# Performance work log

Hardware: AMD Instinct MI355X
Metric: run time of the kernel (lower is better)

## Reference

```python
import jax, jax.numpy as jnp
import numpy as np

B, L, D, H = 4, 2048, 256, 512


def silu_backward(x):
    s = jax.nn.silu(x)
    return s + jax.nn.sigmoid(x) * (1.0 - s)


def setup_inputs() -> dict:
    key = jax.random.key(0)
    ks = jax.random.split(key, 12)
    sc = 0.02
    return {
        "x": jax.random.normal(ks[0], (B, L, D), jnp.float32),
        "W1": jax.random.normal(ks[1], (B, H, D), jnp.float32) * sc,
        "W2": jax.random.normal(ks[2], (B, D, H), jnp.float32) * sc,
        "Wq": jax.random.normal(ks[3], (D, D), jnp.float32) * sc,
        "bq": jnp.zeros((D,), jnp.float32),
        "Wk": jax.random.normal(ks[4], (D, D), jnp.float32) * sc,
        "bk": jnp.zeros((D,), jnp.float32),
        "Wv": jax.random.normal(ks[5], (D, D), jnp.float32) * sc,
        "bv": jnp.zeros((D,), jnp.float32),
        "w_lr": jax.random.normal(ks[6], (D,), jnp.float32) * sc,
        "b_lr": jnp.zeros((), jnp.float32),
        "w_wd": jax.random.normal(ks[7], (D,), jnp.float32) * sc,
        "b_wd": jnp.zeros((), jnp.float32),
        "log_base_lr": jnp.asarray(np.log(0.1), jnp.float32),
        "log_base_wd": jnp.asarray(np.log(0.5), jnp.float32),
    }


def reference(x, W1, W2, Wq, bq, Wk, bk, Wv, bv, w_lr, b_lr, w_wd, b_wd, log_base_lr, log_base_wd):
    b, l, d = x.shape
    query = x @ Wq + bq
    key = x @ Wk + bk
    value = x @ Wv + bv
    lr = jnp.exp(log_base_lr) * jax.nn.sigmoid(x @ w_lr + b_lr)          # [b,l]
    log_wd = jnp.log(1.0 - jnp.exp(log_base_wd) * jax.nn.sigmoid(x @ w_wd + b_wd))  # [b,l]

    wd_cross = jnp.exp(jnp.cumsum(log_wd, axis=1))                       # [b,l]
    idx = jnp.arange(l)
    strict_upper = idx[:, None] < idx[None, :]                           # (m, j): j > m
    A = jnp.where(strict_upper[None], log_wd[:, None, :], 0.0)           # [b,m,j]
    wd_inner = jnp.exp(jnp.cumsum(A, axis=2)) * (idx[:, None] <= idx[None, :])[None]  # [b,m,j]

    X1 = key
    Z1 = jnp.einsum('bhd,bld->blh', W1, X1)
    X2 = jax.nn.silu(Z1)
    Z2 = jnp.einsum('bdh,blh->bld', W2, X2)
    grad_Z2 = Z2 - value
    grad_X2 = jnp.einsum('bdh,bld->blh', W2, grad_Z2)
    grad_Z1 = silu_backward(Z1) * grad_X2

    X1_ = query
    mask_X1X1_ = jnp.einsum('bld,bmd->blm', X1, X1_) * wd_inner
    Z1_inner = -jnp.einsum('blh,bl,blm->bmh', grad_Z1, lr, mask_X1X1_)
    Z1_cross = jnp.einsum('bhd,bld,bl->blh', W1, X1_, wd_cross)
    Z1_ = Z1_inner + Z1_cross

    W1_next = (-jnp.einsum('blh,bl,bld->bhd', grad_Z1, lr * wd_inner[:, :, -1], X1)
               + W1 * wd_cross[:, -1][:, None, None])

    X2_ = jax.nn.silu(Z1_)
    mask_X2X2_ = jnp.einsum('blh,bmh->blm', X2, X2_) * wd_inner
    Z2_inner = -jnp.einsum('bld,bl,blm->bmd', grad_Z2, lr, mask_X2X2_)
    Z2_cross = jnp.einsum('bdh,blh,bl->bld', W2, X2_, wd_cross)
    Z2_ = Z2_inner + Z2_cross

    W2_next = (-jnp.einsum('bld,bl,blh->bdh', grad_Z2, lr * wd_inner[:, :, -1], X2)
               + W2 * wd_cross[:, -1][:, None, None])

    return (Z2_, W1_next, W2_next)
```

## Files before the change

kernel.cpp:

```cpp
#include <hip/hip_runtime.h>

typedef __bf16 bf16;
typedef __bf16 bf16x8 __attribute__((ext_vector_type(8)));
typedef __bf16 bf16x4 __attribute__((ext_vector_type(4)));
typedef float  f32x4  __attribute__((ext_vector_type(4)));

#define SB 72
#define CUTOFF -18.0

__device__ __forceinline__ float silu_f(float x){
  float s = 1.f/(1.f+__expf(-x));
  return x*s;
}
__device__ __forceinline__ float silu_bwd_f(float x){
  float s = 1.f/(1.f+__expf(-x));
  float si = x*s;
  return si + s*(1.f-si);
}

struct MArgs {
  const bf16* A; const bf16* B;
  long sA, sB;
  int lda, ldb;
  int M, N, K;
  int mode;
  float* Cf; long sCf;
  bf16*  Cb; long sCb;
  bf16*  Cb2; long sCb2;
  bf16*  Ct;  long sCt;  int ldct;
  bf16*  Ct2; long sCt2;
  int ldc;
  const float* auxf; int ldax; long sAuxf;
  const bf16*  auxb; long sAuxb;
  const float* rowv; long sRowv;
  const float* rowv2; long sRowv2;
  const double* cd;  long sCd;
  const float* clp;  long sClp;
  bf16* Q; bf16* Ko; float* Vo; const float* bqkv;
};

template<int TM>
__device__ __forceinline__ void gemm_body(const MArgs& g, int bm, int bn, int bz)
{
  constexpr int TTP = (TM==64) ? 72 : 136;
  __shared__ __align__(16) bf16 sh[(TM+64)*SB];
  bf16* As = sh;
  bf16* Bs = sh + TM*SB;

  const int row0 = bm*TM, col0 = bn*64;
  constexpr int NI  = TM/32;
  constexpr int TPR = 256/TM;
  constexpr int EPR = 64/TPR;
  constexpr int NCH = EPR/8;

  const bf16* A = g.A + (long)bz*g.sA;
  const bf16* B = g.B + (long)bz*g.sB;
  const double* cd = g.cd ? g.cd + (long)bz*g.sCd : (const double*)0;
  float* Cf = g.Cf ? g.Cf + (long)bz*g.sCf : (float*)0;
  bf16* Cb  = g.Cb ? g.Cb + (long)bz*g.sCb : (bf16*)0;
  bf16* Cb2 = g.Cb2 ? g.Cb2 + (long)bz*g.sCb2 : (bf16*)0;
  bf16* Ct  = g.Ct ? g.Ct + (long)bz*g.sCt : (bf16*)0;
  bf16* Ct2 = g.Ct2 ? g.Ct2 + (long)bz*g.sCt2 : (bf16*)0;
  const float* auxf = g.auxf ? g.auxf + (long)bz*g.sAuxf : (const float*)0;
  const bf16*  auxb = g.auxb ? g.auxb + (long)bz*g.sAuxb : (const bf16*)0;
  const float* rowv = g.rowv ? g.rowv + (long)bz*g.sRowv : (const float*)0;
  const float* rowv2 = g.rowv2 ? g.rowv2 + (long)bz*g.sRowv2 : (const float*)0;

  const int tid = threadIdx.x;
  const int mode = g.mode;
  const int lane = tid & 63;
  const int w = tid >> 6;
  const int wr = (w >> 1) * (TM/2), wc = (w & 1) * 32;
  const int l15 = lane & 15;
  const int quad = lane >> 4;

  f32x4 acc[NI][2];
  #pragma unroll
  for (int i=0;i<NI;i++)
    #pragma unroll
    for (int j=0;j<2;j++)
      #pragma unroll
      for (int r=0;r<4;r++) acc[i][j][r] = 0.f;

  const int rowA = tid / TPR, kA = (tid % TPR) * EPR;
  const int rowB = tid >> 2,  kB = (tid & 3) * 16;

  int klo = 0;
  if (cd) {
    const double cref = cd[g.K-1];
    while (klo + 64 < g.K && (cref - cd[klo+63]) < CUTOFF) klo += 64;
  }

  for (int k0 = klo; k0 < g.K; k0 += 64) {
    {
      const bf16* s = A + (long)(row0+rowA)*g.lda + k0 + kA;
      #pragma unroll
      for (int p=0;p<NCH;p++)
        *(bf16x8*)&As[rowA*SB + kA + p*8] = *(const bf16x8*)(s + p*8);
    }
    {
      const bf16* s = B + (long)(col0+rowB)*g.ldb + k0 + kB;
      *(bf16x8*)&Bs[rowB*SB + kB]     = *(const bf16x8*)s;
      *(bf16x8*)&Bs[rowB*SB + kB + 8] = *(const bf16x8*)(s+8);
    }
    __syncthreads();
    #pragma unroll
    for (int ch=0; ch<2; ch++){
      bf16x8 af[NI], bf2[2];
      #pragma unroll
      for (int i=0;i<NI;i++) af[i]  = *(const bf16x8*)&As[(wr + i*16 + l15)*SB + ch*32 + quad*8];
      #pragma unroll
      for (int j=0;j<2;j++) bf2[j] = *(const bf16x8*)&Bs[(wc + j*16 + l15)*SB + ch*32 + quad*8];
      #pragma unroll
      for (int i=0;i<NI;i++)
        #pragma unroll
        for (int j=0;j<2;j++)
          acc[i][j] = __builtin_amdgcn_mfma_f32_16x16x32_bf16(af[i], bf2[j], acc[i][j], 0, 0, 0);
    }
    __syncthreads();
  }

  float clv = 0.f;
  if (mode == 10) clv = *(g.clp + (long)bz*g.sClp);

  const bool hasT = (TM==64) ? (mode==1 || mode==2 || mode==3)
                             : (mode==11 && col0 >= 256 && col0 < 512);

  #pragma unroll
  for (int i=0;i<NI;i++){
    const int rb = row0 + wr + i*16 + quad*4;
    const int rloc = wr + i*16 + quad*4;
    #pragma unroll
    for (int j=0;j<2;j++){
      const int c = col0 + wc + j*16 + l15;
      const int cloc = wc + j*16 + l15;
      bf16 tv[4], tv2[4]; bool doT = false, doT2 = false;
      #pragma unroll
      for (int reg=0; reg<4; reg++){
        const int r = rb + reg;
        float v = acc[i][j][reg];
        const long co = (long)r*g.ldc + c;
        switch (mode) {
          case 1: {
            Cb[co]  = (bf16)v;
            float sv = silu_f(v);
            Cb2[co] = (bf16)sv;
            tv[reg] = (bf16)(sv * rowv[r]); doT = true;
          } break;
          case 2: {
            bf16 o = (bf16)(v - auxf[(long)r*g.ldax + c]);
            Cb[co] = o; tv[reg] = o; doT = true;
          } break;
          case 3: {
            float v3 = silu_bwd_f((float)auxb[(long)r*g.ldax + c]) * v * rowv[r];
            tv[reg]  = (bf16)v3;
            tv2[reg] = (bf16)(v3 * rowv2[r]);
            doT = true; doT2 = true;
          } break;
          case 10: {
            Cf[co] = v + auxf[(long)r*g.ldax + c]*clv;
          } break;
          case 11: {
            float o = v + g.bqkv[c];
            if (c < 256)      g.Q [(long)r*256 + c]       = (bf16)o;
            else if (c < 512) { g.Ko[(long)r*256 + (c-256)] = (bf16)o; tv[reg] = (bf16)o; doT = true; }
            else              g.Vo[(long)r*256 + (c-512)] = o;
          } break;
        }
      }
      if (hasT && doT) {
        bf16x4 t4 = { tv[0], tv[1], tv[2], tv[3] };
        *(bf16x4*)&sh[cloc*TTP + rloc] = t4;
        if (doT2) {
          bf16x4 t4b = { tv2[0], tv2[1], tv2[2], tv2[3] };
          *(bf16x4*)&sh[64*72 + cloc*TTP + rloc] = t4b;
        }
      }
    }
  }

  if (hasT) {
    __syncthreads();
    if constexpr (TM == 64) {
      const int cl = tid >> 2, rl = (tid & 3)*16;
      bf16x8 u0 = *(const bf16x8*)&sh[cl*72 + rl];
      bf16x8 u1 = *(const bf16x8*)&sh[cl*72 + rl + 8];
      bf16* d = Ct + (long)(col0+cl)*g.ldct + row0 + rl;
      *(bf16x8*)d       = u0;
      *(bf16x8*)(d + 8) = u1;
      if (mode == 3) {
        bf16x8 v0 = *(const bf16x8*)&sh[64*72 + cl*72 + rl];
        bf16x8 v1 = *(const bf16x8*)&sh[64*72 + cl*72 + rl + 8];
        bf16* d2 = Ct2 + (long)(col0+cl)*g.ldct + row0 + rl;
        *(bf16x8*)d2       = v0;
        *(bf16x8*)(d2 + 8) = v1;
      }
    } else {
      const int cl = tid >> 2, rl = (tid & 3)*32;
      const int b = row0 / g.ldct, l0r = row0 % g.ldct;
      bf16* d = Ct + (long)b*g.sCt + (long)(col0-256+cl)*g.ldct + l0r + rl;
      #pragma unroll
      for (int p=0;p<4;p++)
        *(bf16x8*)(d + p*8) = *(const bf16x8*)&sh[cl*136 + rl + p*8];
    }
  }
}

__global__ __launch_bounds__(256)
void mfma_gemm128(MArgs g){ gemm_body<128>(g, blockIdx.x, blockIdx.y, blockIdx.z); }

__global__ __launch_bounds__(256)
void mfma_gemm64(MArgs g){ gemm_body<64>(g, blockIdx.x, blockIdx.y, blockIdx.z); }

__global__ __launch_bounds__(256)
void wnext_gemm(MArgs g1, MArgs g2){
  const int z = blockIdx.z;
  const MArgs& g = (z < 4) ? g1 : g2;
  const int bz = z & 3;
  if ((int)blockIdx.x*128 >= g.M || (int)blockIdx.y*64 >= g.N) return;
  gemm_body<128>(g, blockIdx.x, blockIdx.y, bz);
}

struct PArgs {
  const bf16 *A, *B1;
  long sA, sB1;
  const double* cd; long sCd;
  const float* lrv; long sLr;
  bf16* P;
};

template<int KS64, int ISLR>
__global__ __launch_bounds__(256)
void pgen(PArgs g)
{
  const int mt = blockIdx.x, slot = blockIdx.y, bz = blockIdx.z;
  const int m0 = mt*64;
  const int l0 = (m0 & ~127) - slot*128;
  if (l0 < 0) return;
  const double* cd = g.cd + (long)bz*g.sCd;
  const int lref = (l0+127 < m0) ? (l0+127) : m0;
  if (cd[m0] - cd[lref] < CUTOFF) return;

  const int K1 = KS64*64;
  const bf16* A  = g.A  + (long)bz*g.sA;
  const bf16* B1 = g.B1 + (long)bz*g.sB1;
  const float* lrv = ISLR ? (g.lrv + (long)bz*g.sLr) : (const float*)0;

  const int tid = threadIdx.x;
  const int lane = tid & 63, w = tid >> 6;
  const int wr = (w>>1)*32, wc = (w&1)*64;
  const int l15 = lane & 15, quad = lane >> 4;
  const int rowA = tid >> 2, kA = (tid & 3) * 16;
  const int rowB = tid >> 1, kB = (tid & 1) * 32;

  __shared__ __align__(16) bf16 As[64*SB];
  __shared__ __align__(16) bf16 Bs[128*SB];

  f32x4 O[2][4];
  #pragma unroll
  for (int i=0;i<2;i++)
    #pragma unroll
    for (int j=0;j<4;j++)
      #pragma unroll
      for (int r=0;r<4;r++) O[i][j][r] = 0.f;

  for (int ks=0; ks<KS64; ks++){
    const int k0 = ks*64;
    {
      const bf16* s = A + (long)(m0+rowA)*K1 + k0 + kA;
      *(bf16x8*)&As[rowA*SB + kA]     = *(const bf16x8*)s;
      *(bf16x8*)&As[rowA*SB + kA + 8] = *(const bf16x8*)(s+8);
    }
    {
      const bf16* s = B1 + (long)(l0+rowB)*K1 + k0 + kB;
      #pragma unroll
      for (int p=0;p<4;p++) *(bf16x8*)&Bs[rowB*SB + kB + p*8] = *(const bf16x8*)(s + p*8);
    }
    __syncthreads();
    #pragma unroll
    for (int ch=0; ch<2; ch++){
      bf16x8 af[2], bfr[4];
      #pragma unroll
      for (int i=0;i<2;i++) af[i]  = *(const bf16x8*)&As[(wr + i*16 + l15)*SB + ch*32 + quad*8];
      #pragma unroll
      for (int j=0;j<4;j++) bfr[j] = *(const bf16x8*)&Bs[(wc + j*16 + l15)*SB + ch*32 + quad*8];
      #pragma unroll
      for (int i=0;i<2;i++)
        #pragma unroll
        for (int j=0;j<4;j++)
          O[i][j] = __builtin_amdgcn_mfma_f32_16x16x32_bf16(af[i], bfr[j], O[i][j], 0, 0, 0);
    }
    __syncthreads();
  }

  bf16* Pt = g.P + (((long)bz*32 + mt)*3 + slot) * (64*128);
  float cl[4], lv[4];
  #pragma unroll
  for (int j=0;j<4;j++){
    const int l = l0 + wc + j*16 + l15;
    cl[j] = (float)cd[l];
    if (ISLR) lv[j] = lrv[l];
  }
  #pragma unroll
  for (int i=0;i<2;i++)
    #pragma unroll
    for (int reg=0; reg<4; reg++){
      const int mloc = wr + i*16 + quad*4 + reg;
      const int m = m0 + mloc;
      const float cm = (float)cd[m];
      #pragma unroll
      for (int j=0;j<4;j++){
        const int lloc = wc + j*16 + l15;
        const int l = l0 + lloc;
        float v = -O[i][j][reg] * __expf(cm - cl[j]);
        if (ISLR) v *= lv[j];
        if (l > m) v = 0.f;
        Pt[mloc*128 + lloc] = (bf16)v;
      }
    }
}

struct CArgs {
  const bf16 *A, *W, *P, *B2;
  long sA, sW, sB2;
  int ldb2;
  const double* cd; long sCd;
  const float* wdc; long sWdc;
  float* Cf; long sCf;
  bf16* Cb; long sCb;
  int ldc;
};

template<int KS64, int SILU, int ZSPLIT>
__global__ __launch_bounds__(256)
void cons(CArgs g)
{
  const int mt = blockIdx.x;
  const int m0 = mt*64, n0 = blockIdx.y*64;
  const int bz   = ZSPLIT ? (blockIdx.z >> 1) : blockIdx.z;
  const int half = ZSPLIT ? (blockIdx.z & 1)  : 0;
  const int K1 = KS64*64;
  const bf16* A  = g.A  + (long)bz*g.sA;
  const bf16* W  = g.W  + (long)bz*g.sW;
  const bf16* B2 = g.B2 + (long)bz*g.sB2;
  const double* cd = g.cd + (long)bz*g.sCd;
  const float* wdc = g.wdc + (long)bz*g.sWdc;

  const int tid = threadIdx.x;
  const int lane = tid & 63, w = tid >> 6;
  const int wr = (w>>1)*32, wc = (w&1)*32;
  const int l15 = lane & 15, quad = lane >> 4;
  const int rowA = tid >> 2, kA = (tid & 3) * 16;

  bool alive[3];
  int nalive = 0;
  #pragma unroll
  for (int s=0;s<3;s++){
    const int l0 = (m0 & ~127) - s*128;
    bool a = (l0 >= 0);
    if (a) {
      const int lref = (l0+127 < m0) ? (l0+127) : m0;
      a = (cd[m0] - cd[lref] >= CUTOFF);
    }
    alive[s] = a; nalive += a ? 1 : 0;
  }
  if (ZSPLIT && half == 1 && nalive == 0) return;

  __shared__ __align__(16) bf16 As[64*SB];
  __shared__ __align__(16) bf16 Bs[64*SB];

  f32x4 O[2][2];
  #pragma unroll
  for (int i=0;i<2;i++)
    #pragma unroll
    for (int j=0;j<2;j++)
      #pragma unroll
      for (int r=0;r<4;r++) O[i][j][r] = 0.f;

  if (half == 0) {
    for (int ks=0; ks<KS64; ks++){
      const int k0 = ks*64;
      {
        const bf16* s = A + (long)(m0+rowA)*K1 + k0 + kA;
        *(bf16x8*)&As[rowA*SB + kA]     = *(const bf16x8*)s;
        *(bf16x8*)&As[rowA*SB + kA + 8] = *(const bf16x8*)(s+8);
      }
      {
        const bf16* s = W + (long)(n0+rowA)*K1 + k0 + kA;
        *(bf16x8*)&Bs[rowA*SB + kA]     = *(const bf16x8*)s;
        *(bf16x8*)&Bs[rowA*SB + kA + 8] = *(const bf16x8*)(s+8);
      }
      __syncthreads();
      #pragma unroll
      for (int ch=0; ch<2; ch++){
        bf16x8 af[2], bfr[2];
        #pragma unroll
        for (int i=0;i<2;i++) af[i]  = *(const bf16x8*)&As[(wr + i*16 + l15)*SB + ch*32 + quad*8];
        #pragma unroll
        for (int j=0;j<2;j++) bfr[j] = *(const bf16x8*)&Bs[(wc + j*16 + l15)*SB + ch*32 + quad*8];
        #pragma unroll
        for (int i=0;i<2;i++)
          #pragma unroll
          for (int j=0;j<2;j++)
            O[i][j] = __builtin_amdgcn_mfma_f32_16x16x32_bf16(af[i], bfr[j], O[i][j], 0, 0, 0);
      }
      __syncthreads();
    }
    #pragma unroll
    for (int i=0;i<2;i++)
      #pragma unroll
      for (int reg=0; reg<4; reg++){
        const float s = wdc[m0 + wr + i*16 + quad*4 + reg];
        #pragma unroll
        for (int j=0;j<2;j++) O[i][j][reg] *= s;
      }
  }

  if (!ZSPLIT || half == 1) {
    for (int s=0; s<3; s++){
      if (!alive[s]) continue;
      const int l0 = (m0 & ~127) - s*128;
      const bf16* Pt = g.P + (((long)bz*32 + mt)*3 + s) * (64*128);
      for (int hk=0; hk<2; hk++){
        {
          const bf16* sp = Pt + (long)rowA*128 + hk*64 + kA;
          *(bf16x8*)&As[rowA*SB + kA]     = *(const bf16x8*)sp;
          *(bf16x8*)&As[rowA*SB + kA + 8] = *(const bf16x8*)(sp+8);
        }
        {
          const bf16* sp = B2 + (long)(n0+rowA)*g.ldb2 + l0 + hk*64 + kA;
          *(bf16x8*)&Bs[rowA*SB + kA]     = *(const bf16x8*)sp;
          *(bf16x8*)&Bs[rowA*SB + kA + 8] = *(const bf16x8*)(sp+8);
        }
        __syncthreads();
        #pragma unroll
        for (int ch=0; ch<2; ch++){
          bf16x8 af[2], bfr[2];
          #pragma unroll
          for (int i=0;i<2;i++) af[i]  = *(const bf16x8*)&As[(wr + i*16 + l15)*SB + ch*32 + quad*8];
          #pragma unroll
          for (int j=0;j<2;j++) bfr[j] = *(const bf16x8*)&Bs[(wc + j*16 + l15)*SB + ch*32 + quad*8];
          #pragma unroll
          for (int i=0;i<2;i++)
            #pragma unroll
            for (int j=0;j<2;j++)
              O[i][j] = __builtin_amdgcn_mfma_f32_16x16x32_bf16(af[i], bfr[j], O[i][j], 0, 0, 0);
        }
        __syncthreads();
      }
    }
  }

  #pragma unroll
  for (int i=0;i<2;i++){
    const int rb = m0 + wr + i*16 + quad*4;
    #pragma unroll
    for (int j=0;j<2;j++){
      const int c = n0 + wc + j*16 + l15;
      #pragma unroll
      for (int reg=0; reg<4; reg++){
        const long co = (long)(rb+reg)*g.ldc + c;
        if (ZSPLIT)     unsafeAtomicAdd(&g.Cf[(long)bz*g.sCf + co], O[i][j][reg]);
        else if (SILU)  g.Cb[(long)bz*g.sCb + co] = (bf16)silu_f(O[i][j][reg]);
        else            g.Cf[(long)bz*g.sCf + co] = O[i][j][reg];
      }
    }
  }
}

struct FrontArgs {
  const float *x, *W1, *W2, *Wq, *Wk, *Wv;
  bf16 *xb, *W1b, *W2b, *Wqkvt, *W2t;
  float* out0;
  const float *wlr, *blr, *wwd, *bwd, *lbl, *lbw;
  float *lr, *lw;
  long LD4, HD4, HD;
};

__global__ __launch_bounds__(256)
void front_kernel(FrontArgs f)
{
  __shared__ bf16 t[64][72];
  const int bid = blockIdx.x;
  const int tid = threadIdx.x;

  if (bid < 1536) {
    const float* src; bf16* dst; long n; long base;
    if (bid < 1024)      { src = f.x;  dst = f.xb;  n = f.LD4; base = (long)bid*2048; }
    else if (bid < 1280) { src = f.W1; dst = f.W1b; n = f.HD4; base = (long)(bid-1024)*2048; }
    else                 { src = f.W2; dst = f.W2b; n = f.HD4; base = (long)(bid-1280)*2048; }
    long i = base + (long)tid*8;
    if (i >= n) return;
    float4 a = *(const float4*)&src[i];
    float4 b = *(const float4*)&src[i+4];
    bf16x8 o;
    o[0]=(bf16)a.x; o[1]=(bf16)a.y; o[2]=(bf16)a.z; o[3]=(bf16)a.w;
    o[4]=(bf16)b.x; o[5]=(bf16)b.y; o[6]=(bf16)b.z; o[7]=(bf16)b.w;
    *(bf16x8*)&dst[i] = o;
    return;
  }
  if (bid < 2560) {
    long i = (long)(bid-1536)*2048 + (long)tid*8;
    float4 z = {0.f,0.f,0.f,0.f};
    *(float4*)&f.out0[i]   = z;
    *(float4*)&f.out0[i+4] = z;
    return;
  }
  if (bid < 2736) {
    const float* ip; bf16* op; int R, C; int r0, c0;
    if (bid < 2608) {
      const int r = bid - 2560;
      const int z = r >> 4, rem = r & 15;
      ip = z==0 ? f.Wq : (z==1 ? f.Wk : f.Wv);
      op = f.Wqkvt + (long)z*256*256;
      R = 256; C = 256;
      r0 = (rem & 3)*64; c0 = (rem >> 2)*64;
    } else {
      const int r = bid - 2608;
      const int b = r >> 5, rem = r & 31;
      ip = f.W2 + (long)b*f.HD;
      op = f.W2t + (long)b*f.HD;
      R = 256; C = 512;
      r0 = (rem & 3)*64; c0 = (rem >> 2)*64;
    }
    const int lr_ = tid>>2, lc = (tid&3)*16;
    #pragma unroll
    for (int q=0;q<4;q++){
      float4 a = *(const float4*)&ip[(long)(r0+lr_)*C + c0+lc + q*4];
      t[lr_][lc+q*4+0] = (bf16)a.x; t[lr_][lc+q*4+1] = (bf16)a.y;
      t[lr_][lc+q*4+2] = (bf16)a.z; t[lr_][lc+q*4+3] = (bf16)a.w;
    }
    __syncthreads();
    const int oc = tid>>2, orr = (tid&3)*16;
    bf16x8 u, v;
    #pragma unroll
    for (int i=0;i<8;i++){ u[i] = t[orr+i][oc]; v[i] = t[orr+8+i][oc]; }
    *(bf16x8*)&op[(long)(c0+oc)*R + r0+orr]   = u;
    *(bf16x8*)&op[(long)(c0+oc)*R + r0+orr+8] = v;
    return;
  }
  {
    const int row  = (bid-2736)*4 + (tid >> 6);
    const int lane = tid & 63;
    const float4 a = ((const float4*)(f.x + (long)row*256))[lane];
    const float4 u = ((const float4*)f.wlr)[lane];
    const float4 w = ((const float4*)f.wwd)[lane];
    float d1 = a.x*u.x + a.y*u.y + a.z*u.z + a.w*u.w;
    float d2 = a.x*w.x + a.y*w.y + a.z*w.z + a.w*w.w;
    #pragma unroll
    for (int off=32; off; off>>=1) {
      d1 += __shfl_down(d1, off);
      d2 += __shfl_down(d2, off);
    }
    if (lane == 0) {
      float s1 = 1.f/(1.f+expf(-(d1 + f.blr[0])));
      f.lr[row] = expf(f.lbl[0]) * s1;
      float s2 = 1.f/(1.f+expf(-(d2 + f.bwd[0])));
      f.lw[row] = logf(1.f - expf(f.lbw[0]) * s2);
    }
  }
}

__global__ __launch_bounds__(256)
void cumsum_kernel(const float* __restrict__ lw, const float* __restrict__ lr,
                   double* __restrict__ cd, float* __restrict__ wdc,
                   float* __restrict__ se1, float* __restrict__ se2, int L,
                   const float* __restrict__ bq, const float* __restrict__ bk,
                   const float* __restrict__ bv, float* __restrict__ bqkv)
{
  const int b = blockIdx.x;
  const int t = threadIdx.x;
  if (b == 4) {
    for (int i = t; i < 768; i += 256)
      bqkv[i] = (i<256) ? bq[i] : ((i<512) ? bk[i-256] : bv[i-512]);
    return;
  }
  const float* lwb = lw + (long)b*L;
  __shared__ double sum_s[256];
  double loc[8];
  double s = 0.0;
  #pragma unroll
  for (int i=0;i<8;i++){ s += (double)lwb[t*8+i]; loc[i] = s; }
  sum_s[t] = s;
  __syncthreads();
  for (int off=1; off<256; off<<=1){
    double v = 0.0;
    if (t >= off) v = sum_s[t-off];
    __syncthreads();
    sum_s[t] += v;
    __syncthreads();
  }
  const double prefix = (t > 0) ? sum_s[t-1] : 0.0;
  const double total  = sum_s[255];
  #pragma unroll
  for (int i=0;i<8;i++){
    double c = prefix + loc[i];
    long idx = (long)b*L + t*8 + i;
    cd[idx]  = c;
    wdc[idx] = (float)exp(c);
    double e = exp(total - c);
    se1[idx] = (float)(-e);
    se2[idx] = (float)(-e) * lr[idx];
  }
}

extern "C" void kernel_launch(void* const* d_in, const int* in_sizes, int n_in,
                              void* d_out, int out_size, void* d_ws, size_t ws_size,
                              hipStream_t stream)
{
  const int Bn = 4, L = 2048, D = 256, H = 512;
  const long LD = (long)L*D, LH = (long)L*H, HD = (long)H*D;

  const float* x   = (const float*)d_in[0];
  const float* W1  = (const float*)d_in[1];
  const float* W2  = (const float*)d_in[2];
  const float* Wq  = (const float*)d_in[3];
  const float* bq  = (const float*)d_in[4];
  const float* Wk  = (const float*)d_in[5];
  const float* bk  = (const float*)d_in[6];
  const float* Wv  = (const float*)d_in[7];
  const float* bv  = (const float*)d_in[8];
  const float* wlr = (const float*)d_in[9];
  const float* blr = (const float*)d_in[10];
  const float* wwd = (const float*)d_in[11];
  const float* bwd = (const float*)d_in[12];
  const float* lbl = (const float*)d_in[13];
  const float* lbw = (const float*)d_in[14];
  (void)in_sizes; (void)n_in; (void)out_size; (void)ws_size;

  float* out0 = (float*)d_out;
  float* out1 = out0 + (long)Bn*LD;
  float* out2 = out1 + (long)Bn*HD;

  char* wsp = (char*)d_ws;
  size_t off = 0;
  auto alloc = [&](size_t bytes)->void*{
    void* p = wsp + off; off += (bytes + 255) & ~(size_t)255; return p;
  };
  bf16* xb    = (bf16*)alloc((size_t)Bn*LD*2);
  bf16* Wqkvt = (bf16*)alloc((size_t)3*D*D*2);
  float* bqkv = (float*)alloc((size_t)3*D*4);
  bf16* W1b  = (bf16*)alloc((size_t)Bn*HD*2);
  bf16* W2b  = (bf16*)alloc((size_t)Bn*HD*2);
  bf16* W2t  = (bf16*)alloc((size_t)Bn*HD*2);
  bf16* Qb   = (bf16*)alloc((size_t)Bn*LD*2);
  bf16* Kb   = (bf16*)alloc((size_t)Bn*LD*2);
  bf16* Kt   = (bf16*)alloc((size_t)Bn*LD*2);
  float* Vf  = (float*)alloc((size_t)Bn*LD*4);
  bf16* Z1b  = (bf16*)alloc((size_t)Bn*LH*2);
  bf16* X2b  = (bf16*)alloc((size_t)Bn*LH*2);
  bf16* X2t  = (bf16*)alloc((size_t)Bn*LH*2);
  bf16* gZb  = (bf16*)alloc((size_t)Bn*LD*2);
  bf16* gZt  = (bf16*)alloc((size_t)Bn*LD*2);
  bf16* A1t  = (bf16*)alloc((size_t)Bn*LH*2);
  bf16* A1s  = (bf16*)alloc((size_t)Bn*LH*2);
  bf16* X2_b = (bf16*)alloc((size_t)Bn*LH*2);
  bf16* Pb1  = (bf16*)alloc((size_t)Bn*32*3*64*128*2);
  bf16* Pb2  = (bf16*)alloc((size_t)Bn*32*3*64*128*2);
  float* lrb = (float*)alloc((size_t)Bn*L*4);
  float* lwb = (float*)alloc((size_t)Bn*L*4);
  float* wdc = (float*)alloc((size_t)Bn*L*4);
  float* se1 = (float*)alloc((size_t)Bn*L*4);
  float* se2 = (float*)alloc((size_t)Bn*L*4);
  double* cdb = (double*)alloc((size_t)Bn*L*8);

  auto run128 = [&](const MArgs& g, int Z){
    dim3 grid(g.M/128, g.N/64, Z);
    mfma_gemm128<<<grid, 256, 0, stream>>>(g);
  };
  auto run64 = [&](const MArgs& g, int Z){
    dim3 grid(g.M/64, g.N/64, Z);
    mfma_gemm64<<<grid, 256, 0, stream>>>(g);
  };

  {
    FrontArgs f{};
    f.x = x; f.W1 = W1; f.W2 = W2; f.Wq = Wq; f.Wk = Wk; f.Wv = Wv;
    f.xb = xb; f.W1b = W1b; f.W2b = W2b; f.Wqkvt = Wqkvt; f.W2t = W2t;
    f.out0 = out0;
    f.wlr = wlr; f.blr = blr; f.wwd = wwd; f.bwd = bwd; f.lbl = lbl; f.lbw = lbw;
    f.lr = lrb; f.lw = lwb;
    f.LD4 = Bn*LD; f.HD4 = Bn*HD; f.HD = HD;
    front_kernel<<<dim3(4784), 256, 0, stream>>>(f);
  }
  cumsum_kernel<<<dim3(5), 256, 0, stream>>>(lwb, lrb, cdb, wdc, se1, se2, L, bq, bk, bv, bqkv);

  {
    MArgs g{}; g.A = xb; g.lda = D; g.B = Wqkvt; g.ldb = D;
    g.M = Bn*L; g.N = 3*D; g.K = D; g.mode = 11; g.ldc = 0;
    g.Q = Qb; g.Ko = Kb; g.Vo = Vf; g.bqkv = bqkv;
    g.Ct = Kt; g.sCt = LD; g.ldct = L;
    run128(g, 1);
  }
  {
    MArgs g{}; g.A = Kb; g.lda = D; g.sA = LD; g.B = W1b; g.ldb = D; g.sB = HD;
    g.M = L; g.N = H; g.K = D; g.mode = 1; g.ldc = H;
    g.Cb = Z1b; g.sCb = LH; g.Cb2 = X2b; g.sCb2 = LH;
    g.Ct = X2t; g.sCt = LH; g.ldct = L;
    g.rowv = se2; g.sRowv = L;
    run64(g, Bn);
  }
  {
    MArgs g{}; g.A = X2b; g.lda = H; g.sA = LH; g.B = W2b; g.ldb = H; g.sB = HD;
    g.M = L; g.N = D; g.K = H; g.mode = 2; g.ldc = D;
    g.auxf = Vf; g.ldax = D; g.sAuxf = LD; g.Cb = gZb; g.sCb = LD;
    g.Ct = gZt; g.sCt = LD; g.ldct = L; run64(g, Bn);
  }
  {
    MArgs g{}; g.A = gZb; g.lda = D; g.sA = LD; g.B = W2t; g.ldb = D; g.sB = HD;
    g.M = L; g.N = H; g.K = D; g.mode = 3; g.ldc = H;
    g.auxb = Z1b; g.ldax = H; g.sAuxb = LH;
    g.rowv = lrb; g.sRowv = L; g.rowv2 = se1; g.sRowv2 = L;
    g.Ct = A1t; g.sCt = LH; g.ldct = L;
    g.Ct2 = A1s; g.sCt2 = LH;
    run64(g, Bn);
  }
  {
    PArgs p{};
    p.A = Qb; p.sA = LD; p.B1 = Kb; p.sB1 = LD;
    p.cd = cdb; p.sCd = L; p.P = Pb1;
    pgen<4,0><<<dim3(32,3,Bn), 256, 0, stream>>>(p);
  }
  {
    CArgs c{};
    c.A = Qb; c.sA = LD; c.W = W1b; c.sW = HD;
    c.P = Pb1; c.B2 = A1t; c.sB2 = LH; c.ldb2 = L;
    c.cd = cdb; c.sCd = L; c.wdc = wdc; c.sWdc = L;
    c.Cb = X2_b; c.sCb = LH; c.ldc = H;
    cons<4,1,0><<<dim3(32, H/64, Bn), 256, 0, stream>>>(c);
  }
  {
    PArgs p{};
    p.A = X2_b; p.sA = LH; p.B1 = X2b; p.sB1 = LH;
    p.cd = cdb; p.sCd = L; p.lrv = lrb; p.sLr = L; p.P = Pb2;
    pgen<8,1><<<dim3(32,3,Bn), 256, 0, stream>>>(p);
  }
  {
    CArgs c{};
    c.A = X2_b; c.sA = LH; c.W = W2b; c.sW = HD;
    c.P = Pb2; c.B2 = gZt; c.sB2 = LD; c.ldb2 = L;
    c.cd = cdb; c.sCd = L; c.wdc = wdc; c.sWdc = L;
    c.Cf = out0; c.sCf = LD; c.ldc = D;
    cons<8,0,1><<<dim3(32, D/64, Bn*2), 256, 0, stream>>>(c);
  }
  {
    MArgs g1{}; g1.A = A1s; g1.lda = L; g1.sA = LH; g1.B = Kt; g1.ldb = L; g1.sB = LD;
    g1.M = H; g1.N = D; g1.K = L; g1.mode = 10; g1.ldc = D;
    g1.cd = cdb; g1.sCd = L;
    g1.auxf = W1; g1.ldax = D; g1.sAuxf = HD; g1.clp = wdc + (L-1); g1.sClp = L;
    g1.Cf = out1; g1.sCf = HD;

    MArgs g2{}; g2.A = gZt; g2.lda = L; g2.sA = LD; g2.B = X2t; g2.ldb = L; g2.sB = LH;
    g2.M = D; g2.N = H; g2.K = L; g2.mode = 10; g2.ldc = H;
    g2.cd = cdb; g2.sCd = L;
    g2.auxf = W2; g2.ldax = H; g2.sAuxf = HD; g2.clp = wdc + (L-1); g2.sClp = L;
    g2.Cf = out2; g2.sCf = HD;

    wnext_gemm<<<dim3(4,8,8), 256, 0, stream>>>(g1, g2);
  }
}
```

Measured before the change: 232.3 us.

## Double-buffer LDS with register prefetch in GEMM kernels and retile W-next GEMM

The GEMM, pgen and cons kernels now use two LDS buffers with register prefetch of the next K-tiles, so global loads overlap MFMA compute and one barrier per step is dropped. The dead-chunk search for the decay cutoff becomes a wavefront ballot in place of a serial loop. The W-next GEMM switches from 128-row to 64-row tiles with double the grid to raise occupancy. In exchange LDS use doubles and register pressure rises, which may cut occupancy, and the reuse of a buffer two steps later relies on the intervening barrier for correctness.

Result: faster. 223.7 us (-3.7%).

```diff
diff --git a/kernel.cpp b/kernel.cpp
--- a/kernel.cpp
+++ b/kernel.cpp
@@ -43,9 +43,8 @@
 __device__ __forceinline__ void gemm_body(const MArgs& g, int bm, int bn, int bz)
 {
   constexpr int TTP = (TM==64) ? 72 : 136;
-  __shared__ __align__(16) bf16 sh[(TM+64)*SB];
-  bf16* As = sh;
-  bf16* Bs = sh + TM*SB;
+  constexpr int BUF = (TM+64)*SB;
+  __shared__ __align__(16) bf16 sh[2*BUF];
 
   const int row0 = bm*TM, col0 = bn*64;
   constexpr int NI  = TM/32;
@@ -88,22 +87,28 @@
   int klo = 0;
   if (cd) {
     const double cref = cd[g.K-1];
-    while (klo + 64 < g.K && (cref - cd[klo+63]) < CUTOFF) klo += 64;
-  }
-
-  for (int k0 = klo; k0 < g.K; k0 += 64) {
-    {
-      const bf16* s = A + (long)(row0+rowA)*g.lda + k0 + kA;
-      #pragma unroll
-      for (int p=0;p<NCH;p++)
-        *(bf16x8*)&As[rowA*SB + kA + p*8] = *(const bf16x8*)(s + p*8);
-    }
-    {
-      const bf16* s = B + (long)(col0+rowB)*g.ldb + k0 + kB;
-      *(bf16x8*)&Bs[rowB*SB + kB]     = *(const bf16x8*)s;
-      *(bf16x8*)&Bs[rowB*SB + kB + 8] = *(const bf16x8*)(s+8);
-    }
-    __syncthreads();
+    const int nch = g.K >> 6;
+    bool dead = (lane < nch-1) && ((cref - cd[lane*64+63]) < CUTOFF);
+    unsigned long long mask = __ballot(dead);
+    klo = (int)__builtin_ctzll(~mask) * 64;
+  }
+
+  const bf16* Abase = A + (long)(row0+rowA)*g.lda + kA;
+  const bf16* Bbase = B + (long)(col0+rowB)*g.ldb + kB;
+
+  bf16x8 paA[NCH], pbA0, pbA1, paB[NCH], pbB0, pbB1;
+  #pragma unroll
+  for (int p=0;p<NCH;p++) paA[p] = *(const bf16x8*)(Abase + klo + p*8);
+  pbA0 = *(const bf16x8*)(Bbase + klo);
+  pbA1 = *(const bf16x8*)(Bbase + klo + 8);
+  if (klo + 64 < g.K) {
+    #pragma unroll
+    for (int p=0;p<NCH;p++) paB[p] = *(const bf16x8*)(Abase + klo + 64 + p*8);
+    pbB0 = *(const bf16x8*)(Bbase + klo + 64);
+    pbB1 = *(const bf16x8*)(Bbase + klo + 64 + 8);
+  }
+
+  auto compute = [&](const bf16* As, const bf16* Bs){
     #pragma unroll
     for (int ch=0; ch<2; ch++){
       bf16x8 af[NI], bf2[2];
@@ -117,7 +122,39 @@
         for (int j=0;j<2;j++)
           acc[i][j] = __builtin_amdgcn_mfma_f32_16x16x32_bf16(af[i], bf2[j], acc[i][j], 0, 0, 0);
     }
-    __syncthreads();
+  };
+
+  for (int k0 = klo; k0 < g.K; k0 += 128) {
+    {
+      bf16* As = sh; bf16* Bs = sh + TM*SB;
+      #pragma unroll
+      for (int p=0;p<NCH;p++) *(bf16x8*)&As[rowA*SB + kA + p*8] = paA[p];
+      *(bf16x8*)&Bs[rowB*SB + kB]     = pbA0;
+      *(bf16x8*)&Bs[rowB*SB + kB + 8] = pbA1;
+      __syncthreads();
+      if (k0 + 128 < g.K) {
+        #pragma unroll
+        for (int p=0;p<NCH;p++) paA[p] = *(const bf16x8*)(Abase + k0 + 128 + p*8);
+        pbA0 = *(const bf16x8*)(Bbase + k0 + 128);
+        pbA1 = *(const bf16x8*)(Bbase + k0 + 128 + 8);
+      }
+      compute(As, Bs);
+    }
+    if (k0 + 64 < g.K) {
+      bf16* As = sh + BUF; bf16* Bs = sh + BUF + TM*SB;
+      #pragma unroll
+      for (int p=0;p<NCH;p++) *(bf16x8*)&As[rowA*SB + kA + p*8] = paB[p];
+      *(bf16x8*)&Bs[rowB*SB + kB]     = pbB0;
+      *(bf16x8*)&Bs[rowB*SB + kB + 8] = pbB1;
+      __syncthreads();
+      if (k0 + 192 < g.K) {
+        #pragma unroll
+        for (int p=0;p<NCH;p++) paB[p] = *(const bf16x8*)(Abase + k0 + 192 + p*8);
+        pbB0 = *(const bf16x8*)(Bbase + k0 + 192);
+        pbB1 = *(const bf16x8*)(Bbase + k0 + 192 + 8);
+      }
+      compute(As, Bs);
+    }
   }
 
   float clv = 0.f;
@@ -217,8 +254,8 @@
   const int z = blockIdx.z;
   const MArgs& g = (z < 4) ? g1 : g2;
   const int bz = z & 3;
-  if ((int)blockIdx.x*128 >= g.M || (int)blockIdx.y*64 >= g.N) return;
-  gemm_body<128>(g, blockIdx.x, blockIdx.y, bz);
+  if ((int)blockIdx.x*64 >= g.M || (int)blockIdx.y*64 >= g.N) return;
+  gemm_body<64>(g, blockIdx.x, blockIdx.y, bz);
 }
 
 struct PArgs {
@@ -253,8 +290,8 @@
   const int rowA = tid >> 2, kA = (tid & 3) * 16;
   const int rowB = tid >> 1, kB = (tid & 1) * 32;
 
-  __shared__ __align__(16) bf16 As[64*SB];
-  __shared__ __align__(16) bf16 Bs[128*SB];
+  constexpr int BUFP = (64+128)*SB;
+  __shared__ __align__(16) bf16 sh[2*BUFP];
 
   f32x4 O[2][4];
   #pragma unroll
@@ -264,19 +301,20 @@
       #pragma unroll
       for (int r=0;r<4;r++) O[i][j][r] = 0.f;
 
-  for (int ks=0; ks<KS64; ks++){
-    const int k0 = ks*64;
-    {
-      const bf16* s = A + (long)(m0+rowA)*K1 + k0 + kA;
-      *(bf16x8*)&As[rowA*SB + kA]     = *(const bf16x8*)s;
-      *(bf16x8*)&As[rowA*SB + kA + 8] = *(const bf16x8*)(s+8);
-    }
-    {
-      const bf16* s = B1 + (long)(l0+rowB)*K1 + k0 + kB;
-      #pragma unroll
-      for (int p=0;p<4;p++) *(bf16x8*)&Bs[rowB*SB + kB + p*8] = *(const bf16x8*)(s + p*8);
-    }
-    __syncthreads();
+  const bf16* Abase = A + (long)(m0+rowA)*K1 + kA;
+  const bf16* Bbase = B1 + (long)(l0+rowB)*K1 + kB;
+
+  bf16x8 paA0, paA1, pbA[4], paB0, paB1, pbB[4];
+  paA0 = *(const bf16x8*)Abase;
+  paA1 = *(const bf16x8*)(Abase + 8);
+  #pragma unroll
+  for (int p=0;p<4;p++) pbA[p] = *(const bf16x8*)(Bbase + p*8);
+  paB0 = *(const bf16x8*)(Abase + 64);
+  paB1 = *(const bf16x8*)(Abase + 64 + 8);
+  #pragma unroll
+  for (int p=0;p<4;p++) pbB[p] = *(const bf16x8*)(Bbase + 64 + p*8);
+
+  auto compute = [&](const bf16* As, const bf16* Bs){
     #pragma unroll
     for (int ch=0; ch<2; ch++){
       bf16x8 af[2], bfr[4];
@@ -290,7 +328,41 @@
         for (int j=0;j<4;j++)
           O[i][j] = __builtin_amdgcn_mfma_f32_16x16x32_bf16(af[i], bfr[j], O[i][j], 0, 0, 0);
     }
-    __syncthreads();
+  };
+
+  for (int ks=0; ks<KS64; ks+=2){
+    {
+      bf16* As = sh; bf16* Bs = sh + 64*SB;
+      *(bf16x8*)&As[rowA*SB + kA]     = paA0;
+      *(bf16x8*)&As[rowA*SB + kA + 8] = paA1;
+      #pragma unroll
+      for (int p=0;p<4;p++) *(bf16x8*)&Bs[rowB*SB + kB + p*8] = pbA[p];
+      __syncthreads();
+      if (ks+2 < KS64) {
+        const int kn = (ks+2)*64;
+        paA0 = *(const bf16x8*)(Abase + kn);
+        paA1 = *(const bf16x8*)(Abase + kn + 8);
+        #pragma unroll
+        for (int p=0;p<4;p++) pbA[p] = *(const bf16x8*)(Bbase + kn + p*8);
+      }
+      compute(As, Bs);
+    }
+    {
+      bf16* As = sh + BUFP; bf16* Bs = sh + BUFP + 64*SB;
+      *(bf16x8*)&As[rowA*SB + kA]     = paB0;
+      *(bf16x8*)&As[rowA*SB + kA + 8] = paB1;
+      #pragma unroll
+      for (int p=0;p<4;p++) *(bf16x8*)&Bs[rowB*SB + kB + p*8] = pbB[p];
+      __syncthreads();
+      if (ks+3 < KS64) {
+        const int kn = (ks+3)*64;
+        paB0 = *(const bf16x8*)(Abase + kn);
+        paB1 = *(const bf16x8*)(Abase + kn + 8);
+        #pragma unroll
+        for (int p=0;p<4;p++) pbB[p] = *(const bf16x8*)(Bbase + kn + p*8);
+      }
+      compute(As, Bs);
+    }
   }
 
   bf16* Pt = g.P + (((long)bz*32 + mt)*3 + slot) * (64*128);
@@ -366,8 +438,8 @@
   }
   if (ZSPLIT && half == 1 && nalive == 0) return;
 
-  __shared__ __align__(16) bf16 As[64*SB];
-  __shared__ __align__(16) bf16 Bs[64*SB];
+  constexpr int BUFC = 128*SB;
+  __shared__ __align__(16) bf16 sh[2*BUFC];
 
   f32x4 O[2][2];
   #pragma unroll
@@ -377,34 +449,59 @@
       #pragma unroll
       for (int r=0;r<4;r++) O[i][j][r] = 0.f;
 
+  auto compute = [&](const bf16* As, const bf16* Bs){
+    #pragma unroll
+    for (int ch=0; ch<2; ch++){
+      bf16x8 af[2], bfr[2];
+      #pragma unroll
+      for (int i=0;i<2;i++) af[i]  = *(const bf16x8*)&As[(wr + i*16 + l15)*SB + ch*32 + quad*8];
+      #pragma unroll
+      for (int j=0;j<2;j++) bfr[j] = *(const bf16x8*)&Bs[(wc + j*16 + l15)*SB + ch*32 + quad*8];
+      #pragma unroll
+      for (int i=0;i<2;i++)
+        #pragma unroll
+        for (int j=0;j<2;j++)
+          O[i][j] = __builtin_amdgcn_mfma_f32_16x16x32_bf16(af[i], bfr[j], O[i][j], 0, 0, 0);
+    }
+  };
+
   if (half == 0) {
-    for (int ks=0; ks<KS64; ks++){
-      const int k0 = ks*64;
+    const bf16* Abase = A + (long)(m0+rowA)*K1 + kA;
+    const bf16* Wbase = W + (long)(n0+rowA)*K1 + kA;
+    bf16x8 aA0,aA1,wA0,wA1, aB0,aB1,wB0,wB1;
+    aA0 = *(const bf16x8*)Abase;        aA1 = *(const bf16x8*)(Abase + 8);
+    wA0 = *(const bf16x8*)Wbase;        wA1 = *(const bf16x8*)(Wbase + 8);
+    aB0 = *(const bf16x8*)(Abase + 64); aB1 = *(const bf16x8*)(Abase + 72);
+    wB0 = *(const bf16x8*)(Wbase + 64); wB1 = *(const bf16x8*)(Wbase + 72);
+    for (int ks=0; ks<KS64; ks+=2){
       {
-        const bf16* s = A + (long)(m0+rowA)*K1 + k0 + kA;
-        *(bf16x8*)&As[rowA*SB + kA]     = *(const bf16x8*)s;
-        *(bf16x8*)&As[rowA*SB + kA + 8] = *(const bf16x8*)(s+8);
+        bf16* As = sh; bf16* Bs = sh + 64*SB;
+        *(bf16x8*)&As[rowA*SB + kA]     = aA0;
+        *(bf16x8*)&As[rowA*SB + kA + 8] = aA1;
+        *(bf16x8*)&Bs[rowA*SB + kA]     = wA0;
+        *(bf16x8*)&Bs[rowA*SB + kA + 8] = wA1;
+        __syncthreads();
+        if (ks+2 < KS64) {
+          const int kn = (ks+2)*64;
+          aA0 = *(const bf16x8*)(Abase + kn); aA1 = *(const bf16x8*)(Abase + kn + 8);
+          wA0 = *(const bf16x8*)(Wbase + kn); wA1 = *(const bf16x8*)(Wbase + kn + 8);
+        }
+        compute(As, Bs);
       }
       {
-        const bf16* s = W + (long)(n0+rowA)*K1 + k0 + kA;
-        *(bf16x8*)&Bs[rowA*SB + kA]     = *(const bf16x8*)s;
-        *(bf16x8*)&Bs[rowA*SB + kA + 8] = *(const bf16x8*)(s+8);
-      }
-      __syncthreads();
-      #pragma unroll
-      for (int ch=0; ch<2; ch++){
-        bf16x8 af[2], bfr[2];
-        #pragma unroll
-        for (int i=0;i<2;i++) af[i]  = *(const bf16x8*)&As[(wr + i*16 + l15)*SB + ch*32 + quad*8];
-        #pragma unroll
-        for (int j=0;j<2;j++) bfr[j] = *(const bf16x8*)&Bs[(wc + j*16 + l15)*SB + ch*32 + quad*8];
-        #pragma unroll
-        for (int i=0;i<2;i++)
-          #pragma unroll
-          for (int j=0;j<2;j++)
-            O[i][j] = __builtin_amdgcn_mfma_f32_16x16x32_bf16(af[i], bfr[j], O[i][j], 0, 0, 0);
-      }
-      __syncthreads();
+        bf16* As = sh + BUFC; bf16* Bs = sh + BUFC + 64*SB;
+        *(bf16x8*)&As[rowA*SB + kA]     = aB0;
+        *(bf16x8*)&As[rowA*SB + kA + 8] = aB1;
+        *(bf16x8*)&Bs[rowA*SB + kA]     = wB0;
+        *(bf16x8*)&Bs[rowA*SB + kA + 8] = wB1;
+        __syncthreads();
+        if (ks+3 < KS64) {
+          const int kn = (ks+3)*64;
+          aB0 = *(const bf16x8*)(Abase + kn); aB1 = *(const bf16x8*)(Abase + kn + 8);
+          wB0 = *(const bf16x8*)(Wbase + kn); wB1 = *(const bf16x8*)(Wbase + kn + 8);
+        }
+        compute(As, Bs);
+      }
     }
     #pragma unroll
     for (int i=0;i<2;i++)
@@ -417,36 +514,54 @@
   }
 
   if (!ZSPLIT || half == 1) {
-    for (int s=0; s<3; s++){
-      if (!alive[s]) continue;
-      const int l0 = (m0 & ~127) - s*128;
-      const bf16* Pt = g.P + (((long)bz*32 + mt)*3 + s) * (64*128);
-      for (int hk=0; hk<2; hk++){
+    int s0a=0, s1a=0, s2a=0, na=0;
+    #pragma unroll
+    for (int s=0;s<3;s++) if (alive[s]) { if (na==0) s0a=s; else if (na==1) s1a=s; else s2a=s; na++; }
+    const int nst = na*2;
+    if (nst > 0) {
+      auto Pptr = [&](int t)->const bf16* {
+        const int i = t>>1;
+        const int s = (i==0) ? s0a : ((i==1) ? s1a : s2a);
+        return g.P + (((long)bz*32 + mt)*3 + s)*(64*128) + (long)rowA*128 + (t&1)*64 + kA;
+      };
+      auto Bptr = [&](int t)->const bf16* {
+        const int i = t>>1;
+        const int s = (i==0) ? s0a : ((i==1) ? s1a : s2a);
+        const int l0 = (m0 & ~127) - s*128;
+        return B2 + (long)(n0+rowA)*g.ldb2 + l0 + (t&1)*64 + kA;
+      };
+      bf16x8 pA0,pA1,bA0,bA1, pB0,pB1,bB0,bB1;
+      { const bf16* pp = Pptr(0); pA0 = *(const bf16x8*)pp; pA1 = *(const bf16x8*)(pp+8);
+        const bf16* bb = Bptr(0); bA0 = *(const bf16x8*)bb; bA1 = *(const bf16x8*)(bb+8); }
+      { const bf16* pp = Pptr(1); pB0 = *(const bf16x8*)pp; pB1 = *(const bf16x8*)(pp+8);
+        const bf16* bb = Bptr(1); bB0 = *(const bf16x8*)bb; bB1 = *(const bf16x8*)(bb+8); }
+      for (int t=0; t<nst; t+=2){
         {
-          const bf16* sp = Pt + (long)rowA*128 + hk*64 + kA;
-          *(bf16x8*)&As[rowA*SB + kA]     = *(const bf16x8*)sp;
-          *(bf16x8*)&As[rowA*SB + kA + 8] = *(const bf16x8*)(sp+8);
+          bf16* As = sh; bf16* Bs = sh + 64*SB;
+          *(bf16x8*)&As[rowA*SB + kA]     = pA0;
+          *(bf16x8*)&As[rowA*SB + kA + 8] = pA1;
+          *(bf16x8*)&Bs[rowA*SB + kA]     = bA0;
+          *(bf16x8*)&Bs[rowA*SB + kA + 8] = bA1;
+          __syncthreads();
+          if (t+2 < nst) {
+            const bf16* pp = Pptr(t+2); pA0 = *(const bf16x8*)pp; pA1 = *(const bf16x8*)(pp+8);
+            const bf16* bb = Bptr(t+2); bA0 = *(const bf16x8*)bb; bA1 = *(const bf16x8*)(bb+8);
+          }
+          compute(As, Bs);
         }
         {
-          const bf16* sp = B2 + (long)(n0+rowA)*g.ldb2 + l0 + hk*64 + kA;
-          *(bf16x8*)&Bs[rowA*SB + kA]     = *(const bf16x8*)sp;
-          *(bf16x8*)&Bs[rowA*SB + kA + 8] = *(const bf16x8*)(sp+8);
+          bf16* As = sh + BUFC; bf16* Bs = sh + BUFC + 64*SB;
+          *(bf16x8*)&As[rowA*SB + kA]     = pB0;
+          *(bf16x8*)&As[rowA*SB + kA + 8] = pB1;
+          *(bf16x8*)&Bs[rowA*SB + kA]     = bB0;
+          *(bf16x8*)&Bs[rowA*SB + kA + 8] = bB1;
+          __syncthreads();
+          if (t+3 < nst) {
+            const bf16* pp = Pptr(t+3); pB0 = *(const bf16x8*)pp; pB1 = *(const bf16x8*)(pp+8);
+            const bf16* bb = Bptr(t+3); bB0 = *(const bf16x8*)bb; bB1 = *(const bf16x8*)(bb+8);
+          }
+          compute(As, Bs);
         }
-        __syncthreads();
-        #pragma unroll
-        for (int ch=0; ch<2; ch++){
-          bf16x8 af[2], bfr[2];
-          #pragma unroll
-          for (int i=0;i<2;i++) af[i]  = *(const bf16x8*)&As[(wr + i*16 + l15)*SB + ch*32 + quad*8];
-          #pragma unroll
-          for (int j=0;j<2;j++) bfr[j] = *(const bf16x8*)&Bs[(wc + j*16 + l15)*SB + ch*32 + quad*8];
-          #pragma unroll
-          for (int i=0;i<2;i++)
-            #pragma unroll
-            for (int j=0;j<2;j++)
-              O[i][j] = __builtin_amdgcn_mfma_f32_16x16x32_bf16(af[i], bfr[j], O[i][j], 0, 0, 0);
-        }
-        __syncthreads();
       }
     }
   }
@@ -756,6 +871,6 @@
     g2.auxf = W2; g2.ldax = H; g2.sAuxf = HD; g2.clp = wdc + (L-1); g2.sClp = L;
     g2.Cf = out2; g2.sCf = HD;
 
-    wnext_gemm<<<dim3(4,8,8), 256, 0, stream>>>(g1, g2);
+    wnext_gemm<<<dim3(8,8,8), 256, 0, stream>>>(g1, g2);
   }
 }
```
